# Kernel optimization log

Hardware: AMD Instinct MI355X
Metric: run time of the kernel (lower is better)

Reference implementation:

```python
import jax, jax.numpy as jnp
import numpy as np

OUT_SHAPE = (32, 112, 112, 64)
N_OUT = int(np.prod(OUT_SHAPE))
IN_SHAPE = (32, 56, 56, 64)


def setup_inputs() -> dict:
    key = jax.random.key(0)
    kx, kp = jax.random.split(key)
    x = jax.random.normal(kx, IN_SHAPE, dtype=jnp.float32)
    pos = jax.random.randint(kp, IN_SHAPE, 0, N_OUT, dtype=jnp.int32)
    return {"x": x, "pos": pos}


def reference(x, pos):
    # Max-unpooling: scatter flattened values into a zeroed flat buffer
    # of size prod(out_shape), then reshape to NHWC out_shape.
    flat_x = x.reshape(-1)
    flat_pos = pos.reshape(-1)
    out = jnp.zeros((N_OUT,), dtype=flat_x.dtype).at[flat_pos].set(flat_x)
    return out.reshape(OUT_SHAPE)
```

## Files before the change

### kernel.cpp

```cpp
#include <hip/hip_runtime.h>


#define N_IN   6422528
#define N_OUT  25690112
#define NB1    49
#define NSUB   64
#define NB2    (NB1*NSUB)
#define CAP1   135168
#define CAP2   2560
#define K4BLK  16
#define ENT1_OFF 4096
#define ENT2_OFF (ENT1_OFF + NB1*CAP1*3)
#define WS_NEED  ((size_t)(ENT2_OFF + (size_t)NB2*CAP2*3) * 4)

__global__ __launch_bounds__(256) void part1_kernel(
        const int* __restrict__ pos, const float* __restrict__ x,
        unsigned* __restrict__ ws) {
    __shared__ unsigned hist[NB1], base[NB1], cur[NB1];
    const int per = (N_IN/4) / 1024;
    const int t0 = blockIdx.x * per, t1 = t0 + per;
    for (int i = threadIdx.x; i < NB1; i += 256) hist[i] = 0;
    __syncthreads();
    for (int t = t0 + threadIdx.x; t < t1; t += 256) {
        int4 p = reinterpret_cast<const int4*>(pos)[t];
        atomicAdd(&hist[((unsigned)p.x) >> 19], 1u);
        atomicAdd(&hist[((unsigned)p.y) >> 19], 1u);
        atomicAdd(&hist[((unsigned)p.z) >> 19], 1u);
        atomicAdd(&hist[((unsigned)p.w) >> 19], 1u);
    }
    __syncthreads();
    for (int i = threadIdx.x; i < NB1; i += 256) {
        base[i] = atomicAdd(&ws[i], hist[i]);
        cur[i] = 0;
    }
    __syncthreads();
    for (int t = t0 + threadIdx.x; t < t1; t += 256) {
        int4   p = reinterpret_cast<const int4*>(pos)[t];
        float4 v = reinterpret_cast<const float4*>(x)[t];
        unsigned ordb = 4u * (unsigned)t + 1u;
        #define EMIT(PC, VC, DC) { \
            unsigned b_ = ((unsigned)(PC)) >> 19; \
            unsigned off_ = base[b_] + atomicAdd(&cur[b_], 1u); \
            if (off_ < CAP1) { \
                unsigned* e_ = ws + ENT1_OFF + (b_ * CAP1 + off_) * 3; \
                unsigned vb_ = __float_as_uint(VC); if (!vb_) vb_ = 0x80000000u; \
                e_[0] = (unsigned)(PC); e_[1] = ordb + (DC); e_[2] = vb_; } }
        EMIT(p.x, v.x, 0u) EMIT(p.y, v.y, 1u) EMIT(p.z, v.z, 2u) EMIT(p.w, v.w, 3u)
        #undef EMIT
    }
}

__global__ __launch_bounds__(256) void part2_kernel(unsigned* __restrict__ ws) {
    __shared__ unsigned hist[NSUB], base[NSUB], cur[NSUB];
    const unsigned b1 = blockIdx.x / K4BLK, j = blockIdx.x % K4BLK;
    const unsigned cnt = min(ws[b1], (unsigned)CAP1);
    const unsigned per = (cnt + K4BLK - 1) / K4BLK;
    const unsigned lo = j * per, hi = min(lo + per, cnt);
    const unsigned* e1 = ws + ENT1_OFF + b1 * CAP1 * 3;
    for (int i = threadIdx.x; i < NSUB; i += 256) hist[i] = 0;
    __syncthreads();
    for (unsigned e = lo + threadIdx.x; e < hi; e += 256)
        atomicAdd(&hist[(e1[e*3] >> 13) & (NSUB-1)], 1u);
    __syncthreads();
    for (int i = threadIdx.x; i < NSUB; i += 256) {
        base[i] = atomicAdd(&ws[64 + b1 * NSUB + i], hist[i]);
        cur[i] = 0;
    }
    __syncthreads();
    for (unsigned e = lo + threadIdx.x; e < hi; e += 256) {
        unsigned pz = e1[e*3], od = e1[e*3+1], vb = e1[e*3+2];
        unsigned sb = (pz >> 13) & (NSUB-1);
        unsigned off = base[sb] + atomicAdd(&cur[sb], 1u);
        if (off < CAP2) {
            unsigned* e2 = ws + ENT2_OFF + ((size_t)(b1 * NSUB + sb) * CAP2 + off) * 3;
            e2[0] = pz; e2[1] = od; e2[2] = vb;
        }
    }
}

__global__ __launch_bounds__(256) void resolve_lds_kernel(
        const unsigned* __restrict__ ws, float* __restrict__ out) {
    __shared__ unsigned long long slots[8192];
    const unsigned sb = blockIdx.x;
    const unsigned cnt = min(ws[64 + sb], (unsigned)CAP2);
    const unsigned* e2 = ws + ENT2_OFF + (size_t)sb * CAP2 * 3;
    for (int s = threadIdx.x; s < 8192; s += 256) slots[s] = 0ull;
    __syncthreads();
    for (unsigned e = threadIdx.x; e < cnt; e += 256) {
        unsigned pz = e2[e*3], od = e2[e*3+1], vb = e2[e*3+2];
        atomicMax(&slots[pz & 8191u],
                  ((unsigned long long)od << 32) | (unsigned long long)vb);
    }
    __syncthreads();
    float* ob = out + (size_t)sb * 8192;
    for (int s = threadIdx.x; s < 8192; s += 256)
        ob[s] = __uint_as_float((unsigned)slots[s]);
}

__global__ __launch_bounds__(256) void scatter_idx_kernel(
        const int* __restrict__ pos, int* __restrict__ winner) {
    const int n4 = N_IN / 4;
    int stride = gridDim.x * blockDim.x;
    for (int i = blockIdx.x * blockDim.x + threadIdx.x; i < n4; i += stride) {
        int4 p = reinterpret_cast<const int4*>(pos)[i];
        int b = i * 4;
        atomicMax(&winner[p.x], b + 0); atomicMax(&winner[p.y], b + 1);
        atomicMax(&winner[p.z], b + 2); atomicMax(&winner[p.w], b + 3);
    }
}
__global__ __launch_bounds__(256) void resolve_kernel(
        const float* __restrict__ x, float* __restrict__ out) {
    const int n4 = N_OUT / 4;
    int stride = gridDim.x * blockDim.x;
    for (int i = blockIdx.x * blockDim.x + threadIdx.x; i < n4; i += stride) {
        int4 v = reinterpret_cast<const int4*>(out)[i];
        float4 r;
        r.x = (v.x < 0) ? 0.0f : x[v.x]; r.y = (v.y < 0) ? 0.0f : x[v.y];
        r.z = (v.z < 0) ? 0.0f : x[v.z]; r.w = (v.w < 0) ? 0.0f : x[v.w];
        reinterpret_cast<float4*>(out)[i] = r;
    }
}

extern "C" void kernel_launch(void* const* d_in, const int* in_sizes, int n_in,
                              void* d_out, int out_size, void* d_ws, size_t ws_size,
                              hipStream_t stream) {
    const float* x  = (const float*)d_in[0];
    const int*  pos = (const int*)d_in[1];
    float* out = (float*)d_out;

    if (ws_size >= WS_NEED) {
        unsigned* ws = (unsigned*)d_ws;
        (void)hipMemsetAsync(d_ws, 0, (64 + NB2) * sizeof(unsigned), stream);
        part1_kernel<<<1024, 256, 0, stream>>>(pos, x, ws);
        part2_kernel<<<NB1 * K4BLK, 256, 0, stream>>>(ws);
        resolve_lds_kernel<<<NB2, 256, 0, stream>>>(ws, out);
    } else {
        (void)hipMemsetAsync(d_out, 0xFF, (size_t)N_OUT * sizeof(int), stream);
        scatter_idx_kernel<<<2048, 256, 0, stream>>>(pos, (int*)d_out);
        resolve_kernel<<<2048, 256, 0, stream>>>(x, out);
    }
}
```

Before: 305.3 us.

## Stage bucket entries in LDS and write coalesced SoA arrays in radix passes

Both partition passes now scatter entries into shared-memory staging buffers sorted by bucket, then write them out contiguously to global memory. The entry layout changes from an interleaved 3-word AoS record to three separate SoA arrays, so loads and stores coalesce. Grid sizes are raised to 2048 blocks for part1 and 64 sub-blocks per bucket for part2 so each block's chunk fits in LDS. The cost is heavier LDS use, which lowers occupancy, and a serial prefix scan done by one thread.

```diff
diff --git a/kernel.cpp b/kernel.cpp
--- a/kernel.cpp
+++ b/kernel.cpp
@@ -5,20 +5,32 @@
 #define N_OUT  25690112
 #define NB1    49
 #define NSUB   64
-#define NB2    (NB1*NSUB)
+#define NB2    3136
 #define CAP1   135168
 #define CAP2   2560
-#define K4BLK  16
-#define ENT1_OFF 4096
-#define ENT2_OFF (ENT1_OFF + NB1*CAP1*3)
-#define WS_NEED  ((size_t)(ENT2_OFF + (size_t)NB2*CAP2*3) * 4)
+#define G1     2048
+#define PER1   784
+#define ST1    3136
+#define K4BLK  64
+#define ST2    2112
+
+#define CUR2_OFF 64
+#define P1_OFF 4096
+#define SZ1 (NB1*CAP1)
+#define O1_OFF (P1_OFF+SZ1)
+#define V1_OFF (O1_OFF+SZ1)
+#define P2_OFF (V1_OFF+SZ1)
+#define SZ2 (NB2*CAP2)
+#define O2_OFF (P2_OFF+SZ2)
+#define V2_OFF (O2_OFF+SZ2)
+#define WS_NEED ((size_t)(V2_OFF+SZ2)*4)
 
 __global__ __launch_bounds__(256) void part1_kernel(
         const int* __restrict__ pos, const float* __restrict__ x,
         unsigned* __restrict__ ws) {
-    __shared__ unsigned hist[NB1], base[NB1], cur[NB1];
-    const int per = (N_IN/4) / 1024;
-    const int t0 = blockIdx.x * per, t1 = t0 + per;
+    __shared__ unsigned hist[NB1], sbase[NB1], gbase[NB1], cur[NB1];
+    __shared__ unsigned sp[ST1], so_[ST1], sv[ST1];
+    const int t0 = blockIdx.x * PER1, t1 = t0 + PER1;
     for (int i = threadIdx.x; i < NB1; i += 256) hist[i] = 0;
     __syncthreads();
     for (int t = t0 + threadIdx.x; t < t1; t += 256) {
@@ -29,9 +41,14 @@
         atomicAdd(&hist[((unsigned)p.w) >> 19], 1u);
     }
     __syncthreads();
-    for (int i = threadIdx.x; i < NB1; i += 256) {
-        base[i] = atomicAdd(&ws[i], hist[i]);
-        cur[i] = 0;
+    if (threadIdx.x == 0) {
+        unsigned run = 0;
+        for (int b = 0; b < NB1; ++b) { sbase[b] = run; run += hist[b]; }
+    }
+    __syncthreads();
+    if (threadIdx.x < NB1) {
+        gbase[threadIdx.x] = atomicAdd(&ws[threadIdx.x], hist[threadIdx.x]);
+        cur[threadIdx.x] = 0;
     }
     __syncthreads();
     for (int t = t0 + threadIdx.x; t < t1; t += 256) {
@@ -40,40 +57,65 @@
         unsigned ordb = 4u * (unsigned)t + 1u;
         #define EMIT(PC, VC, DC) { \
             unsigned b_ = ((unsigned)(PC)) >> 19; \
-            unsigned off_ = base[b_] + atomicAdd(&cur[b_], 1u); \
-            if (off_ < CAP1) { \
-                unsigned* e_ = ws + ENT1_OFF + (b_ * CAP1 + off_) * 3; \
-                unsigned vb_ = __float_as_uint(VC); if (!vb_) vb_ = 0x80000000u; \
-                e_[0] = (unsigned)(PC); e_[1] = ordb + (DC); e_[2] = vb_; } }
+            unsigned s_ = sbase[b_] + atomicAdd(&cur[b_], 1u); \
+            unsigned vb_ = __float_as_uint(VC); if (!vb_) vb_ = 0x80000000u; \
+            sp[s_] = (unsigned)(PC); so_[s_] = ordb + (DC); sv[s_] = vb_; }
         EMIT(p.x, v.x, 0u) EMIT(p.y, v.y, 1u) EMIT(p.z, v.z, 2u) EMIT(p.w, v.w, 3u)
         #undef EMIT
+    }
+    __syncthreads();
+    for (int s = threadIdx.x; s < ST1; s += 256) {
+        unsigned p = sp[s], b = p >> 19;
+        unsigned off = gbase[b] + ((unsigned)s - sbase[b]);
+        if (off < CAP1) {
+            unsigned idx = b * CAP1 + off;
+            ws[P1_OFF + idx] = p;
+            ws[O1_OFF + idx] = so_[s];
+            ws[V1_OFF + idx] = sv[s];
+        }
     }
 }
 
 __global__ __launch_bounds__(256) void part2_kernel(unsigned* __restrict__ ws) {
-    __shared__ unsigned hist[NSUB], base[NSUB], cur[NSUB];
+    __shared__ unsigned hist[NSUB], sbase[NSUB], gbase[NSUB], cur[NSUB];
+    __shared__ unsigned sp[ST2], so_[ST2], sv[ST2];
     const unsigned b1 = blockIdx.x / K4BLK, j = blockIdx.x % K4BLK;
     const unsigned cnt = min(ws[b1], (unsigned)CAP1);
     const unsigned per = (cnt + K4BLK - 1) / K4BLK;
     const unsigned lo = j * per, hi = min(lo + per, cnt);
-    const unsigned* e1 = ws + ENT1_OFF + b1 * CAP1 * 3;
+    const int n = (int)(hi > lo ? hi - lo : 0);
+    const unsigned e0 = b1 * CAP1 + lo;
     for (int i = threadIdx.x; i < NSUB; i += 256) hist[i] = 0;
     __syncthreads();
-    for (unsigned e = lo + threadIdx.x; e < hi; e += 256)
-        atomicAdd(&hist[(e1[e*3] >> 13) & (NSUB-1)], 1u);
+    for (int e = threadIdx.x; e < n; e += 256)
+        atomicAdd(&hist[(ws[P1_OFF + e0 + e] >> 13) & (NSUB-1)], 1u);
     __syncthreads();
-    for (int i = threadIdx.x; i < NSUB; i += 256) {
-        base[i] = atomicAdd(&ws[64 + b1 * NSUB + i], hist[i]);
-        cur[i] = 0;
+    if (threadIdx.x == 0) {
+        unsigned run = 0;
+        for (int b = 0; b < NSUB; ++b) { sbase[b] = run; run += hist[b]; }
     }
     __syncthreads();
-    for (unsigned e = lo + threadIdx.x; e < hi; e += 256) {
-        unsigned pz = e1[e*3], od = e1[e*3+1], vb = e1[e*3+2];
-        unsigned sb = (pz >> 13) & (NSUB-1);
-        unsigned off = base[sb] + atomicAdd(&cur[sb], 1u);
+    if (threadIdx.x < NSUB) {
+        gbase[threadIdx.x] = atomicAdd(&ws[CUR2_OFF + b1 * NSUB + threadIdx.x],
+                                       hist[threadIdx.x]);
+        cur[threadIdx.x] = 0;
+    }
+    __syncthreads();
+    for (int e = threadIdx.x; e < n; e += 256) {
+        unsigned p = ws[P1_OFF + e0 + e];
+        unsigned sb = (p >> 13) & (NSUB-1);
+        unsigned s = sbase[sb] + atomicAdd(&cur[sb], 1u);
+        sp[s] = p; so_[s] = ws[O1_OFF + e0 + e]; sv[s] = ws[V1_OFF + e0 + e];
+    }
+    __syncthreads();
+    for (int s = threadIdx.x; s < n; s += 256) {
+        unsigned p = sp[s], sb = (p >> 13) & (NSUB-1);
+        unsigned off = gbase[sb] + ((unsigned)s - sbase[sb]);
         if (off < CAP2) {
-            unsigned* e2 = ws + ENT2_OFF + ((size_t)(b1 * NSUB + sb) * CAP2 + off) * 3;
-            e2[0] = pz; e2[1] = od; e2[2] = vb;
+            unsigned idx = (b1 * NSUB + sb) * CAP2 + off;
+            ws[P2_OFF + idx] = p;
+            ws[O2_OFF + idx] = so_[s];
+            ws[V2_OFF + idx] = sv[s];
         }
     }
 }
@@ -82,14 +124,15 @@
         const unsigned* __restrict__ ws, float* __restrict__ out) {
     __shared__ unsigned long long slots[8192];
     const unsigned sb = blockIdx.x;
-    const unsigned cnt = min(ws[64 + sb], (unsigned)CAP2);
-    const unsigned* e2 = ws + ENT2_OFF + (size_t)sb * CAP2 * 3;
+    const unsigned cnt = min(ws[CUR2_OFF + sb], (unsigned)CAP2);
+    const unsigned e0 = sb * CAP2;
     for (int s = threadIdx.x; s < 8192; s += 256) slots[s] = 0ull;
     __syncthreads();
     for (unsigned e = threadIdx.x; e < cnt; e += 256) {
-        unsigned pz = e2[e*3], od = e2[e*3+1], vb = e2[e*3+2];
-        atomicMax(&slots[pz & 8191u],
-                  ((unsigned long long)od << 32) | (unsigned long long)vb);
+        unsigned p = ws[P2_OFF + e0 + e];
+        unsigned long long key = ((unsigned long long)ws[O2_OFF + e0 + e] << 32)
+                               | (unsigned long long)ws[V2_OFF + e0 + e];
+        atomicMax(&slots[p & 8191u], key);
     }
     __syncthreads();
     float* ob = out + (size_t)sb * 8192;
@@ -130,8 +173,8 @@
 
     if (ws_size >= WS_NEED) {
         unsigned* ws = (unsigned*)d_ws;
-        (void)hipMemsetAsync(d_ws, 0, (64 + NB2) * sizeof(unsigned), stream);
-        part1_kernel<<<1024, 256, 0, stream>>>(pos, x, ws);
+        (void)hipMemsetAsync(d_ws, 0, P1_OFF * sizeof(unsigned), stream);
+        part1_kernel<<<G1, 256, 0, stream>>>(pos, x, ws);
         part2_kernel<<<NB1 * K4BLK, 256, 0, stream>>>(ws);
         resolve_lds_kernel<<<NB2, 256, 0, stream>>>(ws, out);
     } else {
```

Result: faster. 288.5 us (-5.5%).
